# Kernel optimization log

Hardware: AMD Instinct MI355X
Metric: run time of the kernel (lower is better)

## Reference

```python
import jax, jax.numpy as jnp
import numpy as np

N = 50000          # num_nodes
D = 32             # latent_dim
E2 = 800000        # undirected edge pairs; E = 2*E2 directed edges
STEP = 1.0         # step_size


def setup_inputs() -> dict:
    key = jax.random.key(0)
    k1, k2, k3, k4 = jax.random.split(key, 4)
    # Build a symmetric edge list so every edge (s,t) has its reverse (t,s).
    rng = np.random.default_rng(0)
    src = rng.integers(0, N, size=E2)
    dst = rng.integers(0, N, size=E2)
    edge_index = jnp.asarray(
        np.stack([np.concatenate([src, dst]), np.concatenate([dst, src])]),
        dtype=jnp.int32)                                   # [2, 2*E2]
    # reverse-edge index: edge e in first half <-> e+E2 in second half
    right_idx = jnp.asarray(
        np.concatenate([np.arange(E2) + E2, np.arange(E2)]), dtype=jnp.int32)
    x = jax.random.normal(k1, (N, D), dtype=jnp.float32)
    sheaf_W = jax.random.normal(k2, (1, 2 * D), dtype=jnp.float32) * 0.1
    lin_W = jax.random.normal(k3, (D, D), dtype=jnp.float32) * 0.1
    lin_b = jax.random.normal(k4, (D,), dtype=jnp.float32) * 0.1
    return {"x": x, "sheaf_W": sheaf_W, "lin_W": lin_W, "lin_b": lin_b,
            "edge_index": edge_index, "right_idx": right_idx}


def reference(x, sheaf_W, lin_W, lin_b, edge_index, right_idx):
    row, col = edge_index[0], edge_index[1]
    # predict_restriction_maps: maps = tanh(W_s [x_row ; x_col])  -> [E, 1]
    xe = jnp.concatenate([x[row], x[col]], axis=1)          # [E, 2D]
    maps = jnp.tanh(xe @ sheaf_W.T)                         # [E, 1]
    # build_laplacian (left_idx is identity)
    non_diag = -(maps * maps[right_idx])                    # [E, 1]
    diag_maps = jax.ops.segment_sum(maps ** 2, row, num_segments=N)  # [N, 1]
    d_si = (diag_maps + 1.0) ** -0.5                        # [N, 1]
    norm_maps = d_si[row] * non_diag * d_si[col]            # [E, 1]
    diag = (d_si * diag_maps * d_si)[:, 0]                  # [N]
    # y = linear(x); sparse Laplacian matmul: L @ y
    y = x @ lin_W.T + lin_b                                 # [N, D]
    Ly = diag[:, None] * y + jax.ops.segment_sum(
        norm_maps * y[col], row, num_segments=N)            # [N, D]
    return x - STEP * Ly
```

## Files before the change

kernel.cpp:

```cpp
#include <hip/hip_runtime.h>

#define D 32
#define GBITS 6
#define GSIZE 64
#define BLK 256
#define PPC 2048
#define IPT 8
#define CAP 2560

typedef unsigned long long ull;

static __device__ __forceinline__ unsigned short f2h(float f) {
    _Float16 h = (_Float16)f;
    return __builtin_bit_cast(unsigned short, h);
}
static __device__ __forceinline__ float h2f(unsigned short u) {
    return (float)__builtin_bit_cast(_Float16, u);
}
static __device__ __forceinline__ float ftanh(float u) {
    u = fminf(fmaxf(u, -15.f), 15.f);
    float e = __expf(2.f * u);
    return (e - 1.f) / (e + 1.f);
}

__global__ void k_pre_hist(const float* __restrict__ x,
                           const float* __restrict__ sheafW,
                           const float* __restrict__ linW,
                           const float* __restrict__ linb,
                           const int* __restrict__ ei,
                           float2* __restrict__ ab,
                           float* __restrict__ y,
                           int* __restrict__ bhist,
                           int N, int E2, int E, int nbN, int nblkH, int NBG) {
    if (blockIdx.x < nbN) {
        __shared__ float sW[D * D];
        __shared__ float sB[D];
        __shared__ float sS[2 * D];
        for (int i = threadIdx.x; i < D * D; i += blockDim.x) sW[i] = linW[i];
        if (threadIdx.x < D) sB[threadIdx.x] = linb[threadIdx.x];
        if (threadIdx.x < 2 * D) sS[threadIdx.x] = sheafW[threadIdx.x];
        __syncthreads();

        int n = blockIdx.x * blockDim.x + threadIdx.x;
        if (n >= N) return;

        float xv[D];
        const float4* xp = reinterpret_cast<const float4*>(x + (size_t)n * D);
#pragma unroll
        for (int i = 0; i < D / 4; ++i) {
            float4 v = xp[i];
            xv[4 * i + 0] = v.x; xv[4 * i + 1] = v.y;
            xv[4 * i + 2] = v.z; xv[4 * i + 3] = v.w;
        }

        float av = 0.f, bv = 0.f;
#pragma unroll
        for (int d = 0; d < D; ++d) { av += xv[d] * sS[d]; bv += xv[d] * sS[D + d]; }
        ab[n] = make_float2(av, bv);

        float4* yp = reinterpret_cast<float4*>(y + (size_t)n * D);
#pragma unroll
        for (int j4 = 0; j4 < D / 4; ++j4) {
            float4 o;
#pragma unroll
            for (int jj = 0; jj < 4; ++jj) {
                int j = 4 * j4 + jj;
                float s = sB[j];
#pragma unroll
                for (int d = 0; d < D; ++d) s += xv[d] * sW[j * D + d];
                (&o.x)[jj] = s;
            }
            yp[j4] = o;
        }
    } else {
        __shared__ int hist[1024];
        int blk = blockIdx.x - nbN;
        for (int i = threadIdx.x; i < NBG; i += BLK) hist[i] = 0;
        __syncthreads();
        int base = blk * PPC;
#pragma unroll
        for (int k = 0; k < IPT; ++k) {
            int i = base + k * BLK + threadIdx.x;
            if (i < E2) {
                int s = ei[i];
                int t = ei[E + i];
                atomicAdd(&hist[s >> GBITS], 1);
                atomicAdd(&hist[t >> GBITS], 1);
            }
        }
        __syncthreads();
        for (int i = threadIdx.x; i < NBG; i += BLK)
            bhist[(size_t)i * nblkH + blk] = hist[i];
    }
}

__global__ void k_scanA(int* __restrict__ data, int* __restrict__ bsum, int M) {
    __shared__ int s[256];
    int t = threadIdx.x;
    int i = blockIdx.x * 256 + t;
    int v = (i < M) ? data[i] : 0;
    s[t] = v;
    __syncthreads();
#pragma unroll
    for (int o = 1; o < 256; o <<= 1) {
        int tmp = (t >= o) ? s[t - o] : 0;
        __syncthreads();
        s[t] += tmp;
        __syncthreads();
    }
    if (i < M) data[i] = s[t] - v;
    if (t == 255) bsum[blockIdx.x] = s[255];
}

__global__ void k_scanB(int* __restrict__ data, int NB) {
    __shared__ int s[1024];
    int t = threadIdx.x;
    int per = (NB + 1023) >> 10;
    int beg = t * per;
    int end_ = min(beg + per, NB);
    int sum = 0;
    for (int i = beg; i < end_; ++i) sum += data[i];
    s[t] = sum;
    __syncthreads();
#pragma unroll
    for (int o = 1; o < 1024; o <<= 1) {
        int tmp = (t >= o) ? s[t - o] : 0;
        __syncthreads();
        s[t] += tmp;
        __syncthreads();
    }
    int run = s[t] - sum;
    for (int i = beg; i < end_; ++i) { int v = data[i]; data[i] = run; run += v; }
}

__global__ void k_scatter(const int* __restrict__ ei,
                          const float2* __restrict__ ab,
                          const int* __restrict__ bhist,
                          const int* __restrict__ bsum,
                          ull* __restrict__ binned,
                          int E2, int E, int nblkH, int NBG) {
    __shared__ int cursor[1024];
    for (int i = threadIdx.x; i < NBG; i += BLK) {
        int idx = i * nblkH + blockIdx.x;
        cursor[i] = bhist[idx] + bsum[idx >> 8];
    }
    __syncthreads();
    int base = blockIdx.x * PPC;
#pragma unroll
    for (int k = 0; k < IPT; ++k) {
        int i = base + k * BLK + threadIdx.x;
        if (i < E2) {
            int s = ei[i];
            int t = ei[E + i];
            float2 as = ab[s], at = ab[t];
            float m  = ftanh(as.x + at.y);
            float mr = ftanh(at.x + as.y);
            ull hm = f2h(m), hmr = f2h(mr);
            int pos = atomicAdd(&cursor[s >> GBITS], 1);
            binned[pos] = ((ull)(unsigned)s << 48) | ((ull)(unsigned)t << 32) | (hm << 16) | hmr;
            int pos2 = atomicAdd(&cursor[t >> GBITS], 1);
            binned[pos2] = ((ull)(unsigned)t << 48) | ((ull)(unsigned)s << 32) | (hmr << 16) | hm;
        }
    }
}

__global__ void k_diag_zscale(const ull* __restrict__ binned,
                              const int* __restrict__ bhist,
                              const int* __restrict__ bsum,
                              const float* __restrict__ y,
                              float* __restrict__ dsi, float* __restrict__ diag2,
                              unsigned short* __restrict__ z_h,
                              int E, int nblkH, int NBG, int N) {
    __shared__ float rdiag[GSIZE];
    __shared__ float sds[GSIZE];
    __shared__ int sgs[2];
    int g = blockIdx.x, t = threadIdx.x;
    if (t < GSIZE) rdiag[t] = 0.f;
    if (t < 2) {
        int gg = g + t;
        if (gg < NBG) {
            int idx = gg * nblkH;
            sgs[t] = bhist[idx] + bsum[idx >> 8];
        } else sgs[t] = E;
    }
    __syncthreads();
    int gstart = sgs[0], gend = sgs[1];
    for (int k = gstart + t; k < gend; k += BLK) {
        ull it = binned[k];
        int r = (int)(it >> 48) & (GSIZE - 1);
        float m = h2f((unsigned short)((it >> 16) & 0xFFFF));
        atomicAdd(&rdiag[r], m * m);
    }
    __syncthreads();
    int n0 = g << GBITS;
    if (t < GSIZE) {
        int n = n0 + t;
        if (n < N) {
            float dm = rdiag[t];
            float ds = rsqrtf(dm + 1.0f);
            dsi[n] = ds;
            diag2[n] = dm * ds;
            sds[t] = ds;
        }
    }
    __syncthreads();
    int rows = min(GSIZE, N - n0);
    for (int i = t; i < rows * D; i += BLK) {
        int r = i >> 5;
        size_t p = (size_t)(n0 + r) * D + (i & 31);
        z_h[p] = f2h(sds[r] * y[p]);
    }
}

__global__ __launch_bounds__(512) void k_gather_fused(
        const ull* __restrict__ binned,
        const int* __restrict__ bhist,
        const int* __restrict__ bsum,
        const unsigned short* __restrict__ z_h,
        const float* __restrict__ x,
        const float* __restrict__ dsi,
        const float* __restrict__ diag2,
        float* __restrict__ out,
        int E, int nblkH, int NBG, int N) {
    __shared__ ull raw[CAP];
    __shared__ ull sorted[CAP];
    __shared__ int rhist[GSIZE];
    __shared__ int rbase[GSIZE];
    __shared__ int cur[GSIZE];
    __shared__ float sds[GSIZE];
    __shared__ float sdg[GSIZE];
    __shared__ int ss[GSIZE];
    __shared__ int sgs[2];
    int g = blockIdx.x, t = threadIdx.x;
    int n0 = g << GBITS;
    if (t < GSIZE) {
        rhist[t] = 0;
        int n = n0 + t;
        if (n < N) { sds[t] = dsi[n]; sdg[t] = diag2[n]; }
    }
    if (t < 2) {
        int gg = g + t;
        if (gg < NBG) {
            int idx = gg * nblkH;
            sgs[t] = bhist[idx] + bsum[idx >> 8];
        } else sgs[t] = E;
    }
    __syncthreads();
    int gstart = sgs[0];
    int cnt = min(sgs[1] - gstart, CAP);

    for (int k = t; k < cnt; k += 512) {
        ull it = binned[gstart + k];
        raw[k] = it;
        atomicAdd(&rhist[(int)(it >> 48) & (GSIZE - 1)], 1);
    }
    __syncthreads();

    int v = (t < GSIZE) ? rhist[t] : 0;
    if (t < GSIZE) ss[t] = v;
    __syncthreads();
#pragma unroll
    for (int o = 1; o < GSIZE; o <<= 1) {
        int tmp = 0;
        if (t < GSIZE && t >= o) tmp = ss[t - o];
        __syncthreads();
        if (t < GSIZE) ss[t] += tmp;
        __syncthreads();
    }
    if (t < GSIZE) {
        int ex = ss[t] - v;
        rbase[t] = ex;
        cur[t] = ex;
    }
    __syncthreads();

    for (int k = t; k < cnt; k += 512) {
        ull it = raw[k];
        int r = (int)(it >> 48) & (GSIZE - 1);
        int pos = atomicAdd(&cur[r], 1);
        sorted[pos] = it;
    }
    __syncthreads();

    int hw = t >> 5;
    int lane = t & 31;
    int rows = min(GSIZE, N - n0);
    for (int r = hw; r < rows; r += 16) {
        int beg = rbase[r];
        int end_ = beg + rhist[r];
        float acc = 0.f;
        int k = beg;
        for (; k + 4 <= end_; k += 4) {
            ull i0 = sorted[k + 0];
            ull i1 = sorted[k + 1];
            ull i2 = sorted[k + 2];
            ull i3 = sorted[k + 3];
            int c0 = (int)((i0 >> 32) & 0xFFFF);
            int c1 = (int)((i1 >> 32) & 0xFFFF);
            int c2 = (int)((i2 >> 32) & 0xFFFF);
            int c3 = (int)((i3 >> 32) & 0xFFFF);
            float v0 = h2f(z_h[(size_t)c0 * D + lane]);
            float v1 = h2f(z_h[(size_t)c1 * D + lane]);
            float v2 = h2f(z_h[(size_t)c2 * D + lane]);
            float v3 = h2f(z_h[(size_t)c3 * D + lane]);
            acc += h2f((unsigned short)((i0 >> 16) & 0xFFFF)) * h2f((unsigned short)(i0 & 0xFFFF)) * v0;
            acc += h2f((unsigned short)((i1 >> 16) & 0xFFFF)) * h2f((unsigned short)(i1 & 0xFFFF)) * v1;
            acc += h2f((unsigned short)((i2 >> 16) & 0xFFFF)) * h2f((unsigned short)(i2 & 0xFFFF)) * v2;
            acc += h2f((unsigned short)((i3 >> 16) & 0xFFFF)) * h2f((unsigned short)(i3 & 0xFFFF)) * v3;
        }
        for (; k < end_; ++k) {
            ull it = sorted[k];
            int c = (int)((it >> 32) & 0xFFFF);
            acc += h2f((unsigned short)((it >> 16) & 0xFFFF)) * h2f((unsigned short)(it & 0xFFFF)) *
                   h2f(z_h[(size_t)c * D + lane]);
        }
        size_t p = (size_t)(n0 + r) * D + lane;
        float zown = h2f(z_h[p]);
        out[p] = x[p] - sdg[r] * zown + sds[r] * acc;
    }
}

extern "C" void kernel_launch(void* const* d_in, const int* in_sizes, int n_in,
                              void* d_out, int out_size, void* d_ws, size_t ws_size,
                              hipStream_t stream) {
    const float* x      = (const float*)d_in[0];
    const float* sheafW = (const float*)d_in[1];
    const float* linW   = (const float*)d_in[2];
    const float* linb   = (const float*)d_in[3];
    const int*   ei     = (const int*)d_in[4];

    int N  = in_sizes[0] / D;
    int E  = in_sizes[4] / 2;
    int E2 = E / 2;

    int NBG   = (N + GSIZE - 1) >> GBITS;
    int nblkH = (E2 + PPC - 1) / PPC;
    int MH    = NBG * nblkH;
    int nblkA = (MH + 255) / 256;

    char* wp = (char*)d_ws;
    ull*    binned = (ull*)wp;    wp += (size_t)E * 8;
    float2* ab     = (float2*)wp; wp += (size_t)N * 8;
    float*  y      = (float*)wp;  wp += (size_t)N * D * 4;
    float*  dsi    = (float*)wp;  wp += (size_t)N * 4;
    float*  diag2  = (float*)wp;  wp += (size_t)N * 4;
    unsigned short* z_h = (unsigned short*)wp; wp += (size_t)N * D * 2;
    int*    bhist  = (int*)wp;    wp += (size_t)MH * 4;
    int*    bsumA  = (int*)wp;    wp += (size_t)nblkA * 4;

    float* out = (float*)d_out;

    int nbN = (N + BLK - 1) / BLK;

    k_pre_hist<<<nbN + nblkH, BLK, 0, stream>>>(x, sheafW, linW, linb, ei, ab, y,
                                                bhist, N, E2, E, nbN, nblkH, NBG);
    k_scanA<<<nblkA, 256, 0, stream>>>(bhist, bsumA, MH);
    k_scanB<<<1, 1024, 0, stream>>>(bsumA, nblkA);
    k_scatter<<<nblkH, BLK, 0, stream>>>(ei, ab, bhist, bsumA, binned, E2, E, nblkH, NBG);
    k_diag_zscale<<<NBG, BLK, 0, stream>>>(binned, bhist, bsumA, y, dsi, diag2, z_h,
                                           E, nblkH, NBG, N);
    k_gather_fused<<<NBG, 512, 0, stream>>>(binned, bhist, bsumA, z_h, x, dsi, diag2,
                                            out, E, nblkH, NBG, N);
}
```

Before: 105.0 us.

## Store linear output as fp16 and apply column scaling in gather

```diff
diff --git a/kernel.cpp b/kernel.cpp
--- a/kernel.cpp
+++ b/kernel.cpp
@@ -4,8 +4,8 @@
 #define GBITS 6
 #define GSIZE 64
 #define BLK 256
-#define PPC 2048
-#define IPT 8
+#define PPC 4096
+#define IPT 16
 #define CAP 2560
 
 typedef unsigned long long ull;
@@ -29,7 +29,7 @@
                            const float* __restrict__ linb,
                            const int* __restrict__ ei,
                            float2* __restrict__ ab,
-                           float* __restrict__ y,
+                           unsigned short* __restrict__ y_h,
                            int* __restrict__ bhist,
                            int N, int E2, int E, int nbN, int nblkH, int NBG) {
     if (blockIdx.x < nbN) {
@@ -58,20 +58,18 @@
         for (int d = 0; d < D; ++d) { av += xv[d] * sS[d]; bv += xv[d] * sS[D + d]; }
         ab[n] = make_float2(av, bv);
 
-        float4* yp = reinterpret_cast<float4*>(y + (size_t)n * D);
-#pragma unroll
-        for (int j4 = 0; j4 < D / 4; ++j4) {
-            float4 o;
-#pragma unroll
-            for (int jj = 0; jj < 4; ++jj) {
-                int j = 4 * j4 + jj;
-                float s = sB[j];
-#pragma unroll
-                for (int d = 0; d < D; ++d) s += xv[d] * sW[j * D + d];
-                (&o.x)[jj] = s;
-            }
-            yp[j4] = o;
-        }
+        unsigned short yh[D];
+#pragma unroll
+        for (int j = 0; j < D; ++j) {
+            float s = sB[j];
+#pragma unroll
+            for (int d = 0; d < D; ++d) s += xv[d] * sW[j * D + d];
+            yh[j] = f2h(s);
+        }
+        uint4* dst = reinterpret_cast<uint4*>(y_h + (size_t)n * D);
+        const uint4* src = reinterpret_cast<const uint4*>(yh);
+#pragma unroll
+        for (int q = 0; q < D / 8; ++q) dst[q] = src[q];
     } else {
         __shared__ int hist[1024];
         int blk = blockIdx.x - nbN;
@@ -164,15 +162,12 @@
     }
 }
 
-__global__ void k_diag_zscale(const ull* __restrict__ binned,
-                              const int* __restrict__ bhist,
-                              const int* __restrict__ bsum,
-                              const float* __restrict__ y,
-                              float* __restrict__ dsi, float* __restrict__ diag2,
-                              unsigned short* __restrict__ z_h,
-                              int E, int nblkH, int NBG, int N) {
+__global__ void k_diag(const ull* __restrict__ binned,
+                       const int* __restrict__ bhist,
+                       const int* __restrict__ bsum,
+                       float* __restrict__ dsi, float* __restrict__ diag2,
+                       int E, int nblkH, int NBG, int N) {
     __shared__ float rdiag[GSIZE];
-    __shared__ float sds[GSIZE];
     __shared__ int sgs[2];
     int g = blockIdx.x, t = threadIdx.x;
     if (t < GSIZE) rdiag[t] = 0.f;
@@ -199,16 +194,8 @@
             float dm = rdiag[t];
             float ds = rsqrtf(dm + 1.0f);
             dsi[n] = ds;
-            diag2[n] = dm * ds;
-            sds[t] = ds;
-        }
-    }
-    __syncthreads();
-    int rows = min(GSIZE, N - n0);
-    for (int i = t; i < rows * D; i += BLK) {
-        int r = i >> 5;
-        size_t p = (size_t)(n0 + r) * D + (i & 31);
-        z_h[p] = f2h(sds[r] * y[p]);
+            diag2[n] = dm * ds * ds;
+        }
     }
 }
 
@@ -216,7 +203,7 @@
         const ull* __restrict__ binned,
         const int* __restrict__ bhist,
         const int* __restrict__ bsum,
-        const unsigned short* __restrict__ z_h,
+        const unsigned short* __restrict__ y_h,
         const float* __restrict__ x,
         const float* __restrict__ dsi,
         const float* __restrict__ diag2,
@@ -299,24 +286,24 @@
             int c1 = (int)((i1 >> 32) & 0xFFFF);
             int c2 = (int)((i2 >> 32) & 0xFFFF);
             int c3 = (int)((i3 >> 32) & 0xFFFF);
-            float v0 = h2f(z_h[(size_t)c0 * D + lane]);
-            float v1 = h2f(z_h[(size_t)c1 * D + lane]);
-            float v2 = h2f(z_h[(size_t)c2 * D + lane]);
-            float v3 = h2f(z_h[(size_t)c3 * D + lane]);
-            acc += h2f((unsigned short)((i0 >> 16) & 0xFFFF)) * h2f((unsigned short)(i0 & 0xFFFF)) * v0;
-            acc += h2f((unsigned short)((i1 >> 16) & 0xFFFF)) * h2f((unsigned short)(i1 & 0xFFFF)) * v1;
-            acc += h2f((unsigned short)((i2 >> 16) & 0xFFFF)) * h2f((unsigned short)(i2 & 0xFFFF)) * v2;
-            acc += h2f((unsigned short)((i3 >> 16) & 0xFFFF)) * h2f((unsigned short)(i3 & 0xFFFF)) * v3;
+            float w0 = h2f((unsigned short)((i0 >> 16) & 0xFFFF)) * h2f((unsigned short)(i0 & 0xFFFF)) * dsi[c0];
+            float w1 = h2f((unsigned short)((i1 >> 16) & 0xFFFF)) * h2f((unsigned short)(i1 & 0xFFFF)) * dsi[c1];
+            float w2 = h2f((unsigned short)((i2 >> 16) & 0xFFFF)) * h2f((unsigned short)(i2 & 0xFFFF)) * dsi[c2];
+            float w3 = h2f((unsigned short)((i3 >> 16) & 0xFFFF)) * h2f((unsigned short)(i3 & 0xFFFF)) * dsi[c3];
+            acc += w0 * h2f(y_h[(size_t)c0 * D + lane]);
+            acc += w1 * h2f(y_h[(size_t)c1 * D + lane]);
+            acc += w2 * h2f(y_h[(size_t)c2 * D + lane]);
+            acc += w3 * h2f(y_h[(size_t)c3 * D + lane]);
         }
         for (; k < end_; ++k) {
             ull it = sorted[k];
             int c = (int)((it >> 32) & 0xFFFF);
             acc += h2f((unsigned short)((it >> 16) & 0xFFFF)) * h2f((unsigned short)(it & 0xFFFF)) *
-                   h2f(z_h[(size_t)c * D + lane]);
+                   dsi[c] * h2f(y_h[(size_t)c * D + lane]);
         }
         size_t p = (size_t)(n0 + r) * D + lane;
-        float zown = h2f(z_h[p]);
-        out[p] = x[p] - sdg[r] * zown + sds[r] * acc;
+        float yown = h2f(y_h[p]);
+        out[p] = x[p] - sdg[r] * yown + sds[r] * acc;
     }
 }
 
@@ -341,10 +328,9 @@
     char* wp = (char*)d_ws;
     ull*    binned = (ull*)wp;    wp += (size_t)E * 8;
     float2* ab     = (float2*)wp; wp += (size_t)N * 8;
-    float*  y      = (float*)wp;  wp += (size_t)N * D * 4;
     float*  dsi    = (float*)wp;  wp += (size_t)N * 4;
     float*  diag2  = (float*)wp;  wp += (size_t)N * 4;
-    unsigned short* z_h = (unsigned short*)wp; wp += (size_t)N * D * 2;
+    unsigned short* y_h = (unsigned short*)wp; wp += (size_t)N * D * 2;
     int*    bhist  = (int*)wp;    wp += (size_t)MH * 4;
     int*    bsumA  = (int*)wp;    wp += (size_t)nblkA * 4;
 
@@ -352,13 +338,12 @@
 
     int nbN = (N + BLK - 1) / BLK;
 
-    k_pre_hist<<<nbN + nblkH, BLK, 0, stream>>>(x, sheafW, linW, linb, ei, ab, y,
+    k_pre_hist<<<nbN + nblkH, BLK, 0, stream>>>(x, sheafW, linW, linb, ei, ab, y_h,
                                                 bhist, N, E2, E, nbN, nblkH, NBG);
     k_scanA<<<nblkA, 256, 0, stream>>>(bhist, bsumA, MH);
     k_scanB<<<1, 1024, 0, stream>>>(bsumA, nblkA);
     k_scatter<<<nblkH, BLK, 0, stream>>>(ei, ab, bhist, bsumA, binned, E2, E, nblkH, NBG);
-    k_diag_zscale<<<NBG, BLK, 0, stream>>>(binned, bhist, bsumA, y, dsi, diag2, z_h,
-                                           E, nblkH, NBG, N);
-    k_gather_fused<<<NBG, 512, 0, stream>>>(binned, bhist, bsumA, z_h, x, dsi, diag2,
+    k_diag<<<NBG, BLK, 0, stream>>>(binned, bhist, bsumA, dsi, diag2, E, nblkH, NBG, N);
+    k_gather_fused<<<NBG, 512, 0, stream>>>(binned, bhist, bsumA, y_h, x, dsi, diag2,
                                             out, E, nblkH, NBG, N);
 }
```

Result: faster. 102.1 us (-2.8%).
